# Performance work log

Measured on AMD Instinct MI355X. Metric: run time of the kernel, lower is better.

Reference implementation:

```python
import jax, jax.numpy as jnp
import numpy as np

B = 1024            # batch of CIFAR images (== number of routed tokens, seq_len is 1)
D = 768             # d_model (switch-base-8)
FF = 3072           # d_ff
E = 8               # num experts
L = 12              # encoder layers; odd-indexed layers are sparse MoE (sparse_step=2)
NM = L // 2         # 6 MoE layers and 6 dense FFN layers
NUM_CLASSES = 10


def setup_inputs() -> dict:
    key = jax.random.key(0)
    ks = jax.random.split(key, 12)
    s = 0.02
    return {
        "x": jax.random.normal(ks[0], (B, 3, 32, 32), jnp.float32),
        "proj_w": jax.random.normal(ks[1], (3 * 32 * 32, D), jnp.float32) * s,
        "proj_b": jnp.zeros((D,), jnp.float32),
        "ln1_w": jnp.ones((L, D), jnp.float32),
        "wv": jax.random.normal(ks[2], (L, D, D), jnp.float32) * s,
        "wo": jax.random.normal(ks[3], (L, D, D), jnp.float32) * s,
        "ln2_w": jnp.ones((L, D), jnp.float32),
        "dwi": jax.random.normal(ks[4], (NM, D, FF), jnp.float32) * s,
        "dwo": jax.random.normal(ks[5], (NM, FF, D), jnp.float32) * s,
        "router_w": jax.random.normal(ks[6], (NM, D, E), jnp.float32) * s,
        "ewi": jax.random.normal(ks[7], (NM, E, D, FF), jnp.float32) * s,
        "ewo": jax.random.normal(ks[8], (NM, E, FF, D), jnp.float32) * s,
        "final_ln_w": jnp.ones((D,), jnp.float32),
        "fc_w": jax.random.normal(ks[9], (D, NUM_CLASSES), jnp.float32) * s,
        "fc_b": jnp.zeros((NUM_CLASSES,), jnp.float32),
    }


def rms_norm(h, w, eps=1e-6):
    # T5LayerNorm: RMS norm, no mean subtraction, no bias
    var = jnp.mean(jnp.square(h), axis=-1, keepdims=True)
    return w * (h * jax.lax.rsqrt(var + eps))


def reference(x, proj_w, proj_b, ln1_w, wv, wo, ln2_w, dwi, dwo,
              router_w, ewi, ewo, final_ln_w, fc_w, fc_b):
    # flatten image, project to d_model; unsqueeze(1) in torch -> one token per image,
    # so we keep tokens as [B, D] throughout.
    h = x.reshape(x.shape[0], -1) @ proj_w + proj_b              # [B, D]
    d_i = 0
    m_i = 0
    for layer in range(L):
        # --- self-attention block. seq_len == 1 => softmax over a single key is
        #     identically 1 (for any scores / position bias), so the attention
        #     output is exactly Wo(Wv(x_norm)); q/k projections drop out of the
        #     math (and carry zero gradient).
        n = rms_norm(h, ln1_w[layer])
        h = h + (n @ wv[layer]) @ wo[layer]
        # --- feed-forward block (pre-norm, residual) ---
        n = rms_norm(h, ln2_w[layer])
        if layer % 2 == 1:
            # Switch top-1 MoE. With seq_len==1, token_priority==1 <= expert
            # capacity, so no tokens are ever dropped; every token goes to its
            # argmax expert and is scaled by the router probability.
            logits = n @ router_w[m_i]                           # [B, E]
            probs = jax.nn.softmax(logits, axis=-1)
            top_prob = jnp.max(probs, axis=-1, keepdims=True)    # [B, 1]
            disp = jax.nn.one_hot(jnp.argmax(probs, axis=-1), E, dtype=n.dtype)  # [B, E]
            # dense reference for the sparse dispatch: run every expert, then
            # combine with the one-hot routing mask (same math as gather/scatter)
            hid = jax.nn.relu(jnp.einsum('bd,edf->ebf', n, ewi[m_i]))   # [E, B, FF]
            eout = jnp.einsum('ebf,efd->ebd', hid, ewo[m_i])            # [E, B, D]
            moe = jnp.einsum('ebd,be->bd', eout, disp)                  # [B, D]
            h = h + top_prob * moe
            m_i += 1
        else:
            h = h + jax.nn.relu(n @ dwi[d_i]) @ dwo[d_i]
            d_i += 1
    h = rms_norm(h, final_ln_w)
    return h @ fc_w + fc_b                                      # [B, 10] logits
```

## Files before the change

### kernel.cpp

```cpp
#include <hip/hip_runtime.h>
#include <type_traits>

#define DEV __device__ __forceinline__

typedef _Float16 f16;
typedef __attribute__((ext_vector_type(8))) _Float16 f16x8;
typedef __attribute__((ext_vector_type(4))) float f32x4;

constexpr int NP = 48;

DEV int imin(int a, int b) { return a < b ? a : b; }

DEV int swz(int row, int colByte) { return (row * 128 + colByte) ^ ((row & 7) << 4); }

DEV void split2(float x, float y, unsigned& hi, unsigned& lo) {
  f16 hx = (f16)x, hy = (f16)y;
  f16 lx = (f16)(x - (float)hx), ly = (f16)(y - (float)hy);
  hi = (unsigned)__builtin_bit_cast(unsigned short, hx) |
       ((unsigned)__builtin_bit_cast(unsigned short, hy) << 16);
  lo = (unsigned)__builtin_bit_cast(unsigned short, lx) |
       ((unsigned)__builtin_bit_cast(unsigned short, ly) << 16);
}

DEV void lgkm_barrier() {
  asm volatile("s_waitcnt lgkmcnt(0)" ::: "memory");
  __builtin_amdgcn_s_barrier();
  asm volatile("" ::: "memory");
}

struct GArgs {
  const void* A; const void* Alo;
  const void* B; const void* Blo;
  const float* Hin; float* Hout;
  f16* O16; f16* O16lo;
  const float* rspIn; float* rspOut;
  const float* lnw;
  const int* perm; const int* off;
  int M, K, lda, ldb, ldo;
  long sAz, sBz, sOz;
  long zA, zB, zH;
  int KS;
};

template<int TM,int TN,int WR,int WC,int AM,int BMD,int CM,bool RESID,bool EXPERT>
DEV void gk_body(GArgs a) {
  constexpr int TK = 64;
  constexpr int NT = 256;
  static_assert(WR * WC == 4, "4 waves per block");
  constexpr int WTM = TM / WR, WTN = TN / WC;
  constexpr int FM = WTM / 16, FN = WTN / 16;
  constexpr bool APAIR = (AM == 0);
  constexpr int UA = APAIR ? (TM * (TK / 8)) / NT : (TM * (TK / 4)) / NT;
  constexpr int UB = (BMD == 0) ? (TN * (TK / 8)) / NT : (TN * (TK / 4)) / NT;

  __shared__ __align__(16) f16 As[2 * TM * TK];
  __shared__ __align__(16) f16 Bs[2 * TN * TK];
  __shared__ __align__(16) f16 AsL[2 * TM * TK];
  __shared__ __align__(16) f16 BsL[2 * TN * TK];
  __shared__ float rrlds[(AM == 2 || AM == 3) ? TM : 1];

  const int tid = threadIdx.x;
  const int lane = tid & 63;
  const int wid = tid >> 6;
  const int wr = wid / WC, wc = wid % WC;

  int m0;
  int sEnd = 0x7fffffff;
  const char* Ab = (const char*)a.A;
  const char* AbL = (const char*)a.Alo;
  const char* Bb = (const char*)a.B;
  const char* BbL = (const char*)a.Blo;
  f16* O = a.O16;
  f16* OL = a.O16lo;
  float* HoutP = a.Hout;
  {
    int z = blockIdx.z;
    int e = z / a.KS;
    int kc = z - e * a.KS;
    if constexpr (EXPERT) {
      int o0 = a.off[e], o1 = a.off[e + 1];
      if ((int)blockIdx.y * TM >= o1 - o0) return;
      m0 = o0 + blockIdx.y * TM;
      sEnd = o1;
      Bb += (long)e * a.sBz * 4 + (long)kc * a.zB;
      Ab += (long)kc * a.zA;
      AbL += (long)kc * a.zA;
    } else {
      m0 = blockIdx.y * TM;
      Ab += (long)e * a.sAz * 4 + (long)kc * a.zA;
      AbL += (long)kc * a.zA;
      Bb += (long)e * a.sBz * 4 + (long)kc * a.zB;
    }
    if constexpr (CM == 4) HoutP += (long)kc * a.zH;
  }
  const int n0 = blockIdx.x * TN;

  if constexpr (AM == 2 || AM == 3) {
    if (tid < TM) {
      int s = m0 + tid;
      int row = (AM == 3) ? a.perm[imin(s, a.M - 1)] : imin(s, a.M - 1);
      float ss = 0.f;
      #pragma unroll
      for (int j = 0; j < NP; ++j) ss += a.rspIn[row * NP + j];
      rrlds[tid] = rsqrtf(ss * (1.f / 768.f) + 1e-6f);
    }
  }

  int arow[UA];
  #pragma unroll
  for (int u = 0; u < UA; ++u) {
    int id = tid + u * NT;
    if constexpr (AM == 0) arow[u] = imin(m0 + (id >> 3), a.M - 1);
    else if constexpr (AM == 3) arow[u] = a.perm[imin(m0 + (id >> 4), a.M - 1)];
    else arow[u] = imin(m0 + (id >> 4), a.M - 1);
  }

  using ARt = typename std::conditional<APAIR, int4, float4>::type;
  using BRt = typename std::conditional<BMD == 0, int4, float4>::type;

  auto issueA = [&](ARt* rg, ARt* rl, int k0) {
    #pragma unroll
    for (int u = 0; u < UA; ++u) {
      int id = tid + u * NT;
      if constexpr (APAIR) {
        int kq = id & 7;
        long off = ((long)arow[u] * a.lda + k0 + kq * 8) * 2;
        rg[u] = *(const int4*)(Ab + off);
        rl[u] = *(const int4*)(AbL + off);
      } else {
        int kq = id & 15;
        rg[u] = *(const float4*)(Ab + ((long)arow[u] * a.lda + k0 + kq * 4) * 4);
      }
    }
  };
  auto commitA = [&](ARt* rg, ARt* rl, int k0, int bi) {
    char* base = (char*)As + bi * (TM * 128);
    char* baseL = (char*)AsL + bi * (TM * 128);
    #pragma unroll
    for (int u = 0; u < UA; ++u) {
      int id = tid + u * NT;
      if constexpr (APAIR) {
        int m = id >> 3, kq = id & 7;
        *(int4*)(base + swz(m, kq * 16)) = rg[u];
        *(int4*)(baseL + swz(m, kq * 16)) = rl[u];
      } else {
        int m = id >> 4, kq = id & 15;
        float4 v = *(float4*)&rg[u];
        if constexpr (AM == 2 || AM == 3) {
          float rr = rrlds[m];
          const float* w = a.lnw + k0 + kq * 4;
          v.x *= rr * w[0]; v.y *= rr * w[1]; v.z *= rr * w[2]; v.w *= rr * w[3];
        }
        uint2 ph, pl;
        split2(v.x, v.y, ph.x, pl.x);
        split2(v.z, v.w, ph.y, pl.y);
        *(uint2*)(base + swz(m, kq * 8)) = ph;
        *(uint2*)(baseL + swz(m, kq * 8)) = pl;
      }
    }
  };
  auto issueB = [&](BRt* rg, BRt* rl, int k0) {
    #pragma unroll
    for (int u = 0; u < UB; ++u) {
      int id = tid + u * NT;
      if constexpr (BMD == 0) {
        int n = id >> 3, kq = id & 7;
        long off = ((long)(n0 + n) * a.ldb + k0 + kq * 8) * 2;
        rg[u] = *(const int4*)(Bb + off);
        rl[u] = *(const int4*)(BbL + off);
      } else {
        int n = id % TN, kq = id / TN;
        const float* g = (const float*)Bb;
        #pragma unroll
        for (int i = 0; i < 4; ++i)
          ((float*)&rg[u])[i] = g[(long)(k0 + kq * 4 + i) * a.ldb + (n0 + n)];
      }
    }
  };
  auto commitB = [&](BRt* rg, BRt* rl, int bi) {
    char* base = (char*)Bs + bi * (TN * 128);
    char* baseL = (char*)BsL + bi * (TN * 128);
    #pragma unroll
    for (int u = 0; u < UB; ++u) {
      int id = tid + u * NT;
      if constexpr (BMD == 0) {
        int n = id >> 3, kq = id & 7;
        *(int4*)(base + swz(n, kq * 16)) = rg[u];
        *(int4*)(baseL + swz(n, kq * 16)) = rl[u];
      } else {
        int n = id % TN, kq = id / TN;
        float4 v = *(float4*)&rg[u];
        uint2 ph, pl;
        split2(v.x, v.y, ph.x, pl.x);
        split2(v.z, v.w, ph.y, pl.y);
        *(uint2*)(base + swz(n, kq * 8)) = ph;
        *(uint2*)(baseL + swz(n, kq * 8)) = pl;
      }
    }
  };

  f32x4 acc[FM][FN] = {};
  auto compute = [&](int bi) {
    const char* pA = (const char*)As + bi * (TM * 128);
    const char* pAL = (const char*)AsL + bi * (TM * 128);
    const char* pB = (const char*)Bs + bi * (TN * 128);
    const char* pBL = (const char*)BsL + bi * (TN * 128);
    #pragma unroll
    for (int kk = 0; kk < 2; ++kk) {
      const int col2 = (kk * 32 + (lane >> 4) * 8) * 2;
      f16x8 ah[FM], al[FM], bh[FN], bl[FN];
      #pragma unroll
      for (int i = 0; i < FM; ++i) {
        ah[i] = *(const f16x8*)(pA + swz(wr * WTM + i * 16 + (lane & 15), col2));
        al[i] = *(const f16x8*)(pAL + swz(wr * WTM + i * 16 + (lane & 15), col2));
      }
      #pragma unroll
      for (int j = 0; j < FN; ++j) {
        bh[j] = *(const f16x8*)(pB + swz(wc * WTN + j * 16 + (lane & 15), col2));
        bl[j] = *(const f16x8*)(pBL + swz(wc * WTN + j * 16 + (lane & 15), col2));
      }
      #pragma unroll
      for (int i = 0; i < FM; ++i)
        #pragma unroll
        for (int j = 0; j < FN; ++j) {
          f32x4 t = acc[i][j];
          t = __builtin_amdgcn_mfma_f32_16x16x32_f16(al[i], bh[j], t, 0, 0, 0);
          t = __builtin_amdgcn_mfma_f32_16x16x32_f16(ah[i], bl[j], t, 0, 0, 0);
          t = __builtin_amdgcn_mfma_f32_16x16x32_f16(ah[i], bh[j], t, 0, 0, 0);
          acc[i][j] = t;
        }
    }
  };

  ARt ag0[UA], ag1[UA], ag2[UA], al0[UA], al1[UA], al2[UA];
  BRt bg0[UB], bg1[UB], bg2[UB], bl0[UB], bl1[UB], bl2[UB];
  const int ns = a.K / TK;
  issueA(ag0, al0, 0); issueB(bg0, bl0, 0);
  if (TK < a.K) { issueA(ag1, al1, TK); issueB(bg1, bl1, TK); }
  __syncthreads();
  for (int s = 0; s < ns; s += 6) {
    int k;
    { commitA(ag0, al0, (s + 0) * TK, 0); commitB(bg0, bl0, 0);
      k = (s + 2) * TK; if (k < a.K) { issueA(ag2, al2, k); issueB(bg2, bl2, k); }
      lgkm_barrier(); compute(0); }
    if (s + 1 < ns) {
      commitA(ag1, al1, (s + 1) * TK, 1); commitB(bg1, bl1, 1);
      k = (s + 3) * TK; if (k < a.K) { issueA(ag0, al0, k); issueB(bg0, bl0, k); }
      lgkm_barrier(); compute(1); }
    if (s + 2 < ns) {
      commitA(ag2, al2, (s + 2) * TK, 0); commitB(bg2, bl2, 0);
      k = (s + 4) * TK; if (k < a.K) { issueA(ag1, al1, k); issueB(bg1, bl1, k); }
      lgkm_barrier(); compute(0); }
    if (s + 3 < ns) {
      commitA(ag0, al0, (s + 3) * TK, 1); commitB(bg0, bl0, 1);
      k = (s + 5) * TK; if (k < a.K) { issueA(ag2, al2, k); issueB(bg2, bl2, k); }
      lgkm_barrier(); compute(1); }
    if (s + 4 < ns) {
      commitA(ag1, al1, (s + 4) * TK, 0); commitB(bg1, bl1, 0);
      k = (s + 6) * TK; if (k < a.K) { issueA(ag0, al0, k); issueB(bg0, bl0, k); }
      lgkm_barrier(); compute(0); }
    if (s + 5 < ns) {
      commitA(ag2, al2, (s + 5) * TK, 1); commitB(bg2, bl2, 1);
      k = (s + 7) * TK; if (k < a.K) { issueA(ag1, al1, k); issueB(bg1, bl1, k); }
      lgkm_barrier(); compute(1); }
  }

  const int cr = (lane >> 4) * 4;
  const int cc = lane & 15;
  if constexpr (CM == 0 || CM == 2) {
    #pragma unroll
    for (int i = 0; i < FM; ++i) {
      #pragma unroll
      for (int r = 0; r < 4; ++r) {
        int gm = m0 + wr * WTM + i * 16 + cr + r;
        if (gm >= sEnd) continue;
        #pragma unroll
        for (int j = 0; j < FN; ++j) {
          int gn = n0 + wc * WTN + j * 16 + cc;
          float v = acc[i][j][r];
          if constexpr (CM == 2) v = fmaxf(v, 0.f);
          f16 hv = (f16)v;
          O[(long)gm * a.ldo + gn] = hv;
          OL[(long)gm * a.ldo + gn] = (f16)(v - (float)hv);
        }
      }
    }
  } else if constexpr (CM == 4) {
    #pragma unroll
    for (int i = 0; i < FM; ++i) {
      #pragma unroll
      for (int r = 0; r < 4; ++r) {
        int s = m0 + wr * WTM + i * 16 + cr + r;
        if (s >= sEnd || s >= a.M) continue;
        #pragma unroll
        for (int j = 0; j < FN; ++j) {
          int gn = n0 + wc * WTN + j * 16 + cc;
          HoutP[(long)s * a.ldo + gn] = acc[i][j][r];
        }
      }
    }
  } else {
    #pragma unroll
    for (int i = 0; i < FM; ++i) {
      #pragma unroll
      for (int r = 0; r < 4; ++r) {
        int gm = m0 + wr * WTM + i * 16 + cr + r;
        #pragma unroll
        for (int j = 0; j < FN; ++j) {
          int gn = n0 + wc * WTN + j * 16 + cc;
          float v = acc[i][j][r];
          if constexpr (RESID) v += a.Hin[(long)gm * 768 + gn];
          a.Hout[(long)gm * 768 + gn] = v;
          float ssum = v * v;
          ssum += __shfl_xor(ssum, 1); ssum += __shfl_xor(ssum, 2);
          ssum += __shfl_xor(ssum, 4); ssum += __shfl_xor(ssum, 8);
          if ((lane & 15) == 0)
            a.rspOut[(long)gm * NP + ((n0 + wc * WTN + j * 16) >> 4)] = ssum;
        }
      }
    }
  }
}

__global__ __launch_bounds__(256, 3) void k_wct(GArgs a)  { gk_body<32,64,2,2, 1,1,4, false,false>(a); }
__global__ __launch_bounds__(256, 3) void k_proj(GArgs a) { gk_body<32,64,2,2, 1,1,4, false,false>(a); }
__global__ __launch_bounds__(256, 3) void k_attn(GArgs a) { gk_body<32,32,2,2, 2,1,1, true, false>(a); }
__global__ __launch_bounds__(256, 3) void k_awv(GArgs a)  { gk_body<32,64,2,2, 2,1,0, false,false>(a); }
__global__ __launch_bounds__(256, 3) void k_awo(GArgs a)  { gk_body<32,64,2,2, 0,1,1, true, false>(a); }
__global__ __launch_bounds__(256, 3) void k_ffn1(GArgs a) { gk_body<32,64,2,2, 2,1,2, false,false>(a); }
__global__ __launch_bounds__(256, 3) void k_ffn2(GArgs a) { gk_body<32,64,2,2, 0,1,4, false,false>(a); }
__global__ __launch_bounds__(256, 3) void k_eg1(GArgs a)  { gk_body<64,32,2,2, 3,1,2, false,true>(a); }
__global__ __launch_bounds__(256, 3) void k_eg2(GArgs a)  { gk_body<32,64,2,2, 0,1,4, false,true>(a); }

__global__ __launch_bounds__(256)
void red_k(const float* slab, long sst, const int* perm, const float* prob,
           const float* Hin, const float* bias, float* Hout, float* rsp) {
  int lane = threadIdx.x & 63;
  int s = blockIdx.x * 4 + (threadIdx.x >> 6);
  int row = perm ? perm[s] : s;
  float p = prob ? prob[row] : 1.f;
  #pragma unroll
  for (int p3 = 0; p3 < 3; ++p3) {
    int c = p3 * 256 + lane * 4;
    float4 v = *(const float4*)(slab + (long)s * 768 + c);
    float4 v1 = *(const float4*)(slab + sst + (long)s * 768 + c);
    float4 v2 = *(const float4*)(slab + 2 * sst + (long)s * 768 + c);
    float4 v3 = *(const float4*)(slab + 3 * sst + (long)s * 768 + c);
    v.x = (v.x + v1.x) + (v2.x + v3.x); v.y = (v.y + v1.y) + (v2.y + v3.y);
    v.z = (v.z + v1.z) + (v2.z + v3.z); v.w = (v.w + v1.w) + (v2.w + v3.w);
    v.x *= p; v.y *= p; v.z *= p; v.w *= p;
    if (bias) {
      const float4 b = *(const float4*)(bias + c);
      v.x += b.x; v.y += b.y; v.z += b.z; v.w += b.w;
    }
    if (Hin) {
      const float4 h = *(const float4*)(Hin + (long)row * 768 + c);
      v.x += h.x; v.y += h.y; v.z += h.z; v.w += h.w;
    }
    *(float4*)(Hout + (long)row * 768 + c) = v;
    float ss = v.x * v.x + v.y * v.y + v.z * v.z + v.w * v.w;
    ss += __shfl_xor(ss, 1); ss += __shfl_xor(ss, 2);
    if ((lane & 3) == 0) rsp[(long)row * NP + p3 * 16 + (lane >> 2)] = ss;
  }
}

__global__ __launch_bounds__(256)
void router_k(const float* H, const float* rsp, const float* lnw, const float* rw,
              int* eid, float* prob) {
  int lane = threadIdx.x & 63;
  int row = blockIdx.x * 4 + (threadIdx.x >> 6);
  float ss = 0.f;
  #pragma unroll
  for (int j = 0; j < NP; ++j) ss += rsp[row * NP + j];
  float rr = rsqrtf(ss * (1.f / 768.f) + 1e-6f);
  float le[8] = {0, 0, 0, 0, 0, 0, 0, 0};
  #pragma unroll
  for (int i = 0; i < 12; ++i) {
    int k = i * 64 + lane;
    float n = H[row * 768 + k] * rr * lnw[k];
    const float* w = rw + k * 8;
    float4 w0 = *(const float4*)w, w1 = *(const float4*)(w + 4);
    le[0] += n * w0.x; le[1] += n * w0.y; le[2] += n * w0.z; le[3] += n * w0.w;
    le[4] += n * w1.x; le[5] += n * w1.y; le[6] += n * w1.z; le[7] += n * w1.w;
  }
  #pragma unroll
  for (int m = 1; m < 64; m <<= 1) {
    #pragma unroll
    for (int e = 0; e < 8; ++e) le[e] += __shfl_xor(le[e], m);
  }
  float mx = le[0]; int am = 0;
  #pragma unroll
  for (int e = 1; e < 8; ++e) if (le[e] > mx) { mx = le[e]; am = e; }
  float den = 0.f;
  #pragma unroll
  for (int e = 0; e < 8; ++e) den += expf(le[e] - mx);
  if (lane == 0) { eid[row] = am; prob[row] = 1.f / den; }
}

__global__ __launch_bounds__(256)
void scan_k(const int* eid, int* off, int* perm) {
  __shared__ int cnt[8], c2[8], offs[9];
  int tid = threadIdx.x;
  if (tid < 8) { cnt[tid] = 0; c2[tid] = 0; }
  __syncthreads();
  for (int t = tid; t < 1024; t += 256) atomicAdd(&cnt[eid[t]], 1);
  __syncthreads();
  if (tid == 0) {
    int acc = 0;
    for (int e = 0; e < 8; ++e) { offs[e] = acc; acc += cnt[e]; }
    offs[8] = acc;
    for (int e = 0; e < 9; ++e) off[e] = offs[e];
  }
  __syncthreads();
  for (int t = tid; t < 1024; t += 256) {
    int e = eid[t];
    int r = atomicAdd(&c2[e], 1);
    perm[offs[e] + r] = t;
  }
}

__global__ __launch_bounds__(256)
void fc_k(const float* H, const float* rsp, const float* lnw, const float* fw,
          const float* fb, float* out) {
  int lane = threadIdx.x & 63;
  int row = blockIdx.x * 4 + (threadIdx.x >> 6);
  float ss = 0.f;
  #pragma unroll
  for (int j = 0; j < NP; ++j) ss += rsp[row * NP + j];
  float rr = rsqrtf(ss * (1.f / 768.f) + 1e-6f);
  float acc[10] = {0, 0, 0, 0, 0, 0, 0, 0, 0, 0};
  #pragma unroll
  for (int i = 0; i < 12; ++i) {
    int k = i * 64 + lane;
    float n = H[row * 768 + k] * rr * lnw[k];
    const float* w = fw + k * 10;
    #pragma unroll
    for (int c = 0; c < 10; ++c) acc[c] += n * w[c];
  }
  #pragma unroll
  for (int m = 1; m < 64; m <<= 1) {
    #pragma unroll
    for (int c = 0; c < 10; ++c) acc[c] += __shfl_xor(acc[c], m);
  }
  if (lane == 0) {
    #pragma unroll
    for (int c = 0; c < 10; ++c) out[row * 10 + c] = acc[c] + fb[c];
  }
}

extern "C" void kernel_launch(void* const* d_in, const int* in_sizes, int n_in,
                              void* d_out, int out_size, void* d_ws, size_t ws_size,
                              hipStream_t stream) {
  const float* x     = (const float*)d_in[0];
  const float* projw = (const float*)d_in[1];
  const float* projb = (const float*)d_in[2];
  const float* ln1   = (const float*)d_in[3];
  const float* wvp   = (const float*)d_in[4];
  const float* wop   = (const float*)d_in[5];
  const float* ln2   = (const float*)d_in[6];
  const float* dwi   = (const float*)d_in[7];
  const float* dwo   = (const float*)d_in[8];
  const float* rw    = (const float*)d_in[9];
  const float* ewi   = (const float*)d_in[10];
  const float* ewo   = (const float*)d_in[11];
  const float* flnw  = (const float*)d_in[12];
  const float* fcw   = (const float*)d_in[13];
  const float* fcb   = (const float*)d_in[14];

  char* ws = (char*)d_ws;
  float* hA   = (float*)(ws);
  float* hB   = (float*)(ws + 3145728);
  f16*   hidH = (f16*)(ws + 6291456);
  f16*   hidL = (f16*)(ws + 12582912);
  float* rsp  = (float*)(ws + 18874368);
  int*   eid  = (int*)(ws + 23789568);
  float* prob = (float*)(ws + 23793664);
  int*   perm = (int*)(ws + 23797760);
  int*   off  = (int*)(ws + 23801856);
  float* slab = (float*)(ws + 23802368);
  float* wct  = (float*)(ws + 36385280);
  if (ws_size < 36385280u) return;
  const bool useWct = ws_size >= 64696832u;
  auto slot = [&](int s) { return rsp + (long)s * 1024 * NP; };
  const long SST = 1024 * 768;

  if (useWct) {
    GArgs g{}; g.A = wvp; g.B = wop; g.Hout = wct; g.KS = 12;
    g.M = 768; g.K = 768; g.lda = 768; g.ldb = 768; g.ldo = 768;
    g.zA = (long)589824 * 4; g.zB = (long)589824 * 4; g.zH = 589824;
    k_wct<<<dim3(12,24,12), 256, 0, stream>>>(g);
  }
  {
    GArgs g{}; g.A = x; g.B = projw; g.Hout = slab; g.KS = 4;
    g.M = 1024; g.K = 768; g.lda = 3072; g.ldb = 768; g.ldo = 768;
    g.zA = 768 * 4; g.zB = (long)768 * 768 * 4; g.zH = SST;
    k_proj<<<dim3(12,32,4), 256, 0, stream>>>(g);
    red_k<<<dim3(256), 256, 0, stream>>>(slab, SST, nullptr, nullptr, nullptr, projb, hA, slot(0));
  }
  for (int l = 0; l < 12; ++l) {
    if (useWct) {
      GArgs g{}; g.A = hA; g.B = wct + (long)l * 589824;
      g.Hin = hA; g.Hout = hB; g.KS = 1;
      g.rspIn = slot(2*l); g.rspOut = slot(2*l+1); g.lnw = ln1 + l * 768;
      g.M = 1024; g.K = 768; g.lda = 768; g.ldb = 768;
      k_attn<<<dim3(24,32,1), 256, 0, stream>>>(g);
    } else {
      {
        GArgs g{}; g.A = hA; g.B = wvp + (long)l * 589824;
        g.O16 = hidH; g.O16lo = hidL; g.KS = 1;
        g.rspIn = slot(2*l); g.lnw = ln1 + l * 768;
        g.M = 1024; g.K = 768; g.lda = 768; g.ldb = 768; g.ldo = 768;
        k_awv<<<dim3(12,32,1), 256, 0, stream>>>(g);
      }
      {
        GArgs g{}; g.A = hidH; g.Alo = hidL; g.B = wop + (long)l * 589824;
        g.Hin = hA; g.Hout = hB; g.rspOut = slot(2*l+1); g.KS = 1;
        g.M = 1024; g.K = 768; g.lda = 768; g.ldb = 768;
        k_awo<<<dim3(12,32,1), 256, 0, stream>>>(g);
      }
    }
    if ((l & 1) == 0) {
      int di = l / 2;
      {
        GArgs g{}; g.A = hB; g.B = dwi + (long)di * 768 * 3072;
        g.O16 = hidH; g.O16lo = hidL; g.KS = 1;
        g.rspIn = slot(2*l+1); g.lnw = ln2 + l * 768;
        g.M = 1024; g.K = 768; g.lda = 768; g.ldb = 3072; g.ldo = 3072;
        k_ffn1<<<dim3(48,32,1), 256, 0, stream>>>(g);
      }
      {
        GArgs g{}; g.A = hidH; g.Alo = hidL; g.B = dwo + (long)di * 3072 * 768;
        g.Hout = slab; g.KS = 4;
        g.M = 1024; g.K = 768; g.lda = 3072; g.ldb = 768; g.ldo = 768;
        g.zA = 768 * 2; g.zB = (long)768 * 768 * 4; g.zH = SST;
        k_ffn2<<<dim3(12,32,4), 256, 0, stream>>>(g);
        red_k<<<dim3(256), 256, 0, stream>>>(slab, SST, nullptr, nullptr, hB, nullptr, hA, slot(2*l+2));
      }
    } else {
      int mi = l / 2;
      router_k<<<dim3(256), 256, 0, stream>>>(hB, slot(2*l+1), ln2 + l * 768,
                                              rw + (long)mi * 768 * 8, eid, prob);
      scan_k<<<dim3(1), 256, 0, stream>>>(eid, off, perm);
      {
        GArgs g{}; g.A = hB; g.B = ewi + (long)mi * 8 * 768 * 3072;
        g.O16 = hidH; g.O16lo = hidL; g.perm = perm; g.off = off; g.KS = 1;
        g.rspIn = slot(2*l+1); g.lnw = ln2 + l * 768;
        g.M = 1024; g.K = 768; g.lda = 768; g.ldb = 3072; g.ldo = 3072;
        g.sBz = (long)768 * 3072;
        k_eg1<<<dim3(96,16,8), 256, 0, stream>>>(g);
      }
      {
        GArgs g{}; g.A = hidH; g.Alo = hidL; g.B = ewo + (long)mi * 8 * 3072 * 768;
        g.Hout = slab; g.off = off; g.KS = 4;
        g.M = 1024; g.K = 768; g.lda = 3072; g.ldb = 768; g.ldo = 768;
        g.sBz = (long)3072 * 768; g.zA = 768 * 2; g.zB = (long)768 * 768 * 4; g.zH = SST;
        k_eg2<<<dim3(12,32,32), 256, 0, stream>>>(g);
        red_k<<<dim3(256), 256, 0, stream>>>(slab, SST, perm, prob, hB, nullptr, hA, slot(2*l+2));
      }
    }
  }
  fc_k<<<dim3(256), 256, 0, stream>>>(hA, slot(24), flnw, fcw, fcb, (float*)d_out);
}
```

Baseline: 1.750 ms.

## Drop split-K slabs and fuse reductions, routing scan into GEMM epilogues

The projection, dense FFN2 and expert FFN2 GEMMs no longer use 4-way split-K with a partial-sum slab and a separate red_k reduction. They now run full K in one pass, and bias, router-probability scaling, permuted scatter and residual add are applied directly in the GEMM epilogue. The router and scan kernels are merged into one kernel, where the last block to finish (tracked by an atomic ticket) does the expert histogram and permutation. This removes launches and slab memory traffic. In exchange, the affected GEMMs get 4x fewer blocks with 4x longer K loops, which can hurt occupancy and parallelism on a GPU with many CUs.

```diff
diff --git a/kernel.cpp b/kernel.cpp
--- a/kernel.cpp
+++ b/kernel.cpp
@@ -35,6 +35,7 @@
   f16* O16; f16* O16lo;
   const float* rspIn; float* rspOut;
   const float* lnw;
+  const float* prob; const float* bias;
   const int* perm; const int* off;
   int M, K, lda, ldb, ldo;
   long sAz, sBz, sOz;
@@ -42,7 +43,7 @@
   int KS;
 };
 
-template<int TM,int TN,int WR,int WC,int AM,int BMD,int CM,bool RESID,bool EXPERT>
+template<int TM,int TN,int WR,int WC,int AM,int BMD,int CM,bool RESID,bool BIAS,bool EXPERT>
 DEV void gk_body(GArgs a) {
   constexpr int TK = 64;
   constexpr int NT = 256;
@@ -51,7 +52,7 @@
   constexpr int FM = WTM / 16, FN = WTN / 16;
   constexpr bool APAIR = (AM == 0);
   constexpr int UA = APAIR ? (TM * (TK / 8)) / NT : (TM * (TK / 4)) / NT;
-  constexpr int UB = (BMD == 0) ? (TN * (TK / 8)) / NT : (TN * (TK / 4)) / NT;
+  constexpr int UB = (TN * (TK / 4)) / NT;
 
   __shared__ __align__(16) f16 As[2 * TM * TK];
   __shared__ __align__(16) f16 Bs[2 * TN * TK];
@@ -69,7 +70,6 @@
   const char* Ab = (const char*)a.A;
   const char* AbL = (const char*)a.Alo;
   const char* Bb = (const char*)a.B;
-  const char* BbL = (const char*)a.Blo;
   f16* O = a.O16;
   f16* OL = a.O16lo;
   float* HoutP = a.Hout;
@@ -116,7 +116,7 @@
   }
 
   using ARt = typename std::conditional<APAIR, int4, float4>::type;
-  using BRt = typename std::conditional<BMD == 0, int4, float4>::type;
+  using BRt = float4;
 
   auto issueA = [&](ARt* rg, ARt* rl, int k0) {
     #pragma unroll
@@ -159,43 +159,30 @@
       }
     }
   };
-  auto issueB = [&](BRt* rg, BRt* rl, int k0) {
+  auto issueB = [&](BRt* rg, int k0) {
     #pragma unroll
     for (int u = 0; u < UB; ++u) {
       int id = tid + u * NT;
-      if constexpr (BMD == 0) {
-        int n = id >> 3, kq = id & 7;
-        long off = ((long)(n0 + n) * a.ldb + k0 + kq * 8) * 2;
-        rg[u] = *(const int4*)(Bb + off);
-        rl[u] = *(const int4*)(BbL + off);
-      } else {
-        int n = id % TN, kq = id / TN;
-        const float* g = (const float*)Bb;
-        #pragma unroll
-        for (int i = 0; i < 4; ++i)
-          ((float*)&rg[u])[i] = g[(long)(k0 + kq * 4 + i) * a.ldb + (n0 + n)];
-      }
+      int n = id % TN, kq = id / TN;
+      const float* g = (const float*)Bb;
+      #pragma unroll
+      for (int i = 0; i < 4; ++i)
+        ((float*)&rg[u])[i] = g[(long)(k0 + kq * 4 + i) * a.ldb + (n0 + n)];
     }
   };
-  auto commitB = [&](BRt* rg, BRt* rl, int bi) {
+  auto commitB = [&](BRt* rg, int bi) {
     char* base = (char*)Bs + bi * (TN * 128);
     char* baseL = (char*)BsL + bi * (TN * 128);
     #pragma unroll
     for (int u = 0; u < UB; ++u) {
       int id = tid + u * NT;
-      if constexpr (BMD == 0) {
-        int n = id >> 3, kq = id & 7;
-        *(int4*)(base + swz(n, kq * 16)) = rg[u];
-        *(int4*)(baseL + swz(n, kq * 16)) = rl[u];
-      } else {
-        int n = id % TN, kq = id / TN;
-        float4 v = *(float4*)&rg[u];
-        uint2 ph, pl;
-        split2(v.x, v.y, ph.x, pl.x);
-        split2(v.z, v.w, ph.y, pl.y);
-        *(uint2*)(base + swz(n, kq * 8)) = ph;
-        *(uint2*)(baseL + swz(n, kq * 8)) = pl;
-      }
+      int n = id % TN, kq = id / TN;
+      float4 v = *(float4*)&rg[u];
+      uint2 ph, pl;
+      split2(v.x, v.y, ph.x, pl.x);
+      split2(v.z, v.w, ph.y, pl.y);
+      *(uint2*)(base + swz(n, kq * 8)) = ph;
+      *(uint2*)(baseL + swz(n, kq * 8)) = pl;
     }
   };
 
@@ -233,35 +220,35 @@
   };
 
   ARt ag0[UA], ag1[UA], ag2[UA], al0[UA], al1[UA], al2[UA];
-  BRt bg0[UB], bg1[UB], bg2[UB], bl0[UB], bl1[UB], bl2[UB];
+  BRt bg0[UB], bg1[UB], bg2[UB];
   const int ns = a.K / TK;
-  issueA(ag0, al0, 0); issueB(bg0, bl0, 0);
-  if (TK < a.K) { issueA(ag1, al1, TK); issueB(bg1, bl1, TK); }
+  issueA(ag0, al0, 0); issueB(bg0, 0);
+  if (TK < a.K) { issueA(ag1, al1, TK); issueB(bg1, TK); }
   __syncthreads();
   for (int s = 0; s < ns; s += 6) {
     int k;
-    { commitA(ag0, al0, (s + 0) * TK, 0); commitB(bg0, bl0, 0);
-      k = (s + 2) * TK; if (k < a.K) { issueA(ag2, al2, k); issueB(bg2, bl2, k); }
+    { commitA(ag0, al0, (s + 0) * TK, 0); commitB(bg0, 0);
+      k = (s + 2) * TK; if (k < a.K) { issueA(ag2, al2, k); issueB(bg2, k); }
       lgkm_barrier(); compute(0); }
     if (s + 1 < ns) {
-      commitA(ag1, al1, (s + 1) * TK, 1); commitB(bg1, bl1, 1);
-      k = (s + 3) * TK; if (k < a.K) { issueA(ag0, al0, k); issueB(bg0, bl0, k); }
+      commitA(ag1, al1, (s + 1) * TK, 1); commitB(bg1, 1);
+      k = (s + 3) * TK; if (k < a.K) { issueA(ag0, al0, k); issueB(bg0, k); }
       lgkm_barrier(); compute(1); }
     if (s + 2 < ns) {
-      commitA(ag2, al2, (s + 2) * TK, 0); commitB(bg2, bl2, 0);
-      k = (s + 4) * TK; if (k < a.K) { issueA(ag1, al1, k); issueB(bg1, bl1, k); }
+      commitA(ag2, al2, (s + 2) * TK, 0); commitB(bg2, 0);
+      k = (s + 4) * TK; if (k < a.K) { issueA(ag1, al1, k); issueB(bg1, k); }
       lgkm_barrier(); compute(0); }
     if (s + 3 < ns) {
-      commitA(ag0, al0, (s + 3) * TK, 1); commitB(bg0, bl0, 1);
-      k = (s + 5) * TK; if (k < a.K) { issueA(ag2, al2, k); issueB(bg2, bl2, k); }
+      commitA(ag0, al0, (s + 3) * TK, 1); commitB(bg0, 1);
+      k = (s + 5) * TK; if (k < a.K) { issueA(ag2, al2, k); issueB(bg2, k); }
       lgkm_barrier(); compute(1); }
     if (s + 4 < ns) {
-      commitA(ag1, al1, (s + 4) * TK, 0); commitB(bg1, bl1, 0);
-      k = (s + 6) * TK; if (k < a.K) { issueA(ag0, al0, k); issueB(bg0, bl0, k); }
+      commitA(ag1, al1, (s + 4) * TK, 0); commitB(bg1, 0);
+      k = (s + 6) * TK; if (k < a.K) { issueA(ag0, al0, k); issueB(bg0, k); }
       lgkm_barrier(); compute(0); }
     if (s + 5 < ns) {
-      commitA(ag2, al2, (s + 5) * TK, 1); commitB(bg2, bl2, 1);
-      k = (s + 7) * TK; if (k < a.K) { issueA(ag1, al1, k); issueB(bg1, bl1, k); }
+      commitA(ag2, al2, (s + 5) * TK, 1); commitB(bg2, 1);
+      k = (s + 7) * TK; if (k < a.K) { issueA(ag1, al1, k); issueB(bg1, k); }
       lgkm_barrier(); compute(1); }
   }
 
@@ -304,71 +291,50 @@
     for (int i = 0; i < FM; ++i) {
       #pragma unroll
       for (int r = 0; r < 4; ++r) {
-        int gm = m0 + wr * WTM + i * 16 + cr + r;
+        int s = m0 + wr * WTM + i * 16 + cr + r;
+        int grow = s;
+        float p = 1.f;
+        bool ok = true;
+        if constexpr (CM == 3) {
+          ok = s < sEnd;
+          int t = a.perm[imin(s, a.M - 1)];
+          grow = t;
+          p = a.prob[t];
+        }
         #pragma unroll
         for (int j = 0; j < FN; ++j) {
           int gn = n0 + wc * WTN + j * 16 + cc;
           float v = acc[i][j][r];
-          if constexpr (RESID) v += a.Hin[(long)gm * 768 + gn];
-          a.Hout[(long)gm * 768 + gn] = v;
+          if constexpr (CM == 3) v *= p;
+          if constexpr (BIAS) v += a.bias[gn];
+          if constexpr (RESID) v += a.Hin[(long)grow * 768 + gn];
+          if constexpr (CM == 3) v += a.Hin[(long)grow * 768 + gn];
+          if (ok) a.Hout[(long)grow * 768 + gn] = v;
           float ssum = v * v;
           ssum += __shfl_xor(ssum, 1); ssum += __shfl_xor(ssum, 2);
           ssum += __shfl_xor(ssum, 4); ssum += __shfl_xor(ssum, 8);
-          if ((lane & 15) == 0)
-            a.rspOut[(long)gm * NP + ((n0 + wc * WTN + j * 16) >> 4)] = ssum;
+          if (ok && (lane & 15) == 0)
+            a.rspOut[(long)grow * NP + ((n0 + wc * WTN + j * 16) >> 4)] = ssum;
         }
       }
     }
   }
 }
 
-__global__ __launch_bounds__(256, 3) void k_wct(GArgs a)  { gk_body<32,64,2,2, 1,1,4, false,false>(a); }
-__global__ __launch_bounds__(256, 3) void k_proj(GArgs a) { gk_body<32,64,2,2, 1,1,4, false,false>(a); }
-__global__ __launch_bounds__(256, 3) void k_attn(GArgs a) { gk_body<32,32,2,2, 2,1,1, true, false>(a); }
-__global__ __launch_bounds__(256, 3) void k_awv(GArgs a)  { gk_body<32,64,2,2, 2,1,0, false,false>(a); }
-__global__ __launch_bounds__(256, 3) void k_awo(GArgs a)  { gk_body<32,64,2,2, 0,1,1, true, false>(a); }
-__global__ __launch_bounds__(256, 3) void k_ffn1(GArgs a) { gk_body<32,64,2,2, 2,1,2, false,false>(a); }
-__global__ __launch_bounds__(256, 3) void k_ffn2(GArgs a) { gk_body<32,64,2,2, 0,1,4, false,false>(a); }
-__global__ __launch_bounds__(256, 3) void k_eg1(GArgs a)  { gk_body<64,32,2,2, 3,1,2, false,true>(a); }
-__global__ __launch_bounds__(256, 3) void k_eg2(GArgs a)  { gk_body<32,64,2,2, 0,1,4, false,true>(a); }
+__global__ __launch_bounds__(256, 3) void k_wct(GArgs a)  { gk_body<32,64,2,2, 1,1,4, false,false,false>(a); }
+__global__ __launch_bounds__(256, 3) void k_proj(GArgs a) { gk_body<32,64,2,2, 1,1,1, false,true, false>(a); }
+__global__ __launch_bounds__(256, 3) void k_attn(GArgs a) { gk_body<32,32,2,2, 2,1,1, true, false,false>(a); }
+__global__ __launch_bounds__(256, 3) void k_ffn1(GArgs a) { gk_body<32,64,2,2, 2,1,2, false,false,false>(a); }
+__global__ __launch_bounds__(256, 3) void k_ffn2(GArgs a) { gk_body<32,64,2,2, 0,1,1, true, false,false>(a); }
+__global__ __launch_bounds__(256, 3) void k_eg1(GArgs a)  { gk_body<64,32,2,2, 3,1,2, false,false,true>(a); }
+__global__ __launch_bounds__(256, 3) void k_eg2(GArgs a)  { gk_body<32,64,2,2, 0,1,3, false,false,true>(a); }
 
 __global__ __launch_bounds__(256)
-void red_k(const float* slab, long sst, const int* perm, const float* prob,
-           const float* Hin, const float* bias, float* Hout, float* rsp) {
-  int lane = threadIdx.x & 63;
-  int s = blockIdx.x * 4 + (threadIdx.x >> 6);
-  int row = perm ? perm[s] : s;
-  float p = prob ? prob[row] : 1.f;
-  #pragma unroll
-  for (int p3 = 0; p3 < 3; ++p3) {
-    int c = p3 * 256 + lane * 4;
-    float4 v = *(const float4*)(slab + (long)s * 768 + c);
-    float4 v1 = *(const float4*)(slab + sst + (long)s * 768 + c);
-    float4 v2 = *(const float4*)(slab + 2 * sst + (long)s * 768 + c);
-    float4 v3 = *(const float4*)(slab + 3 * sst + (long)s * 768 + c);
-    v.x = (v.x + v1.x) + (v2.x + v3.x); v.y = (v.y + v1.y) + (v2.y + v3.y);
-    v.z = (v.z + v1.z) + (v2.z + v3.z); v.w = (v.w + v1.w) + (v2.w + v3.w);
-    v.x *= p; v.y *= p; v.z *= p; v.w *= p;
-    if (bias) {
-      const float4 b = *(const float4*)(bias + c);
-      v.x += b.x; v.y += b.y; v.z += b.z; v.w += b.w;
-    }
-    if (Hin) {
-      const float4 h = *(const float4*)(Hin + (long)row * 768 + c);
-      v.x += h.x; v.y += h.y; v.z += h.z; v.w += h.w;
-    }
-    *(float4*)(Hout + (long)row * 768 + c) = v;
-    float ss = v.x * v.x + v.y * v.y + v.z * v.z + v.w * v.w;
-    ss += __shfl_xor(ss, 1); ss += __shfl_xor(ss, 2);
-    if ((lane & 3) == 0) rsp[(long)row * NP + p3 * 16 + (lane >> 2)] = ss;
-  }
-}
-
-__global__ __launch_bounds__(256)
-void router_k(const float* H, const float* rsp, const float* lnw, const float* rw,
-              int* eid, float* prob) {
-  int lane = threadIdx.x & 63;
-  int row = blockIdx.x * 4 + (threadIdx.x >> 6);
+void rs_k(const float* H, const float* rsp, const float* lnw, const float* rw,
+          int* eid, float* prob, int* off, int* perm, int* done) {
+  int tid = threadIdx.x;
+  int lane = tid & 63;
+  int row = blockIdx.x * 4 + (tid >> 6);
   float ss = 0.f;
   #pragma unroll
   for (int j = 0; j < NP; ++j) ss += rsp[row * NP + j];
@@ -388,28 +354,31 @@
     #pragma unroll
     for (int e = 0; e < 8; ++e) le[e] += __shfl_xor(le[e], m);
   }
-  float mx = le[0]; int am = 0;
-  #pragma unroll
-  for (int e = 1; e < 8; ++e) if (le[e] > mx) { mx = le[e]; am = e; }
-  float den = 0.f;
-  #pragma unroll
-  for (int e = 0; e < 8; ++e) den += expf(le[e] - mx);
-  if (lane == 0) { eid[row] = am; prob[row] = 1.f / den; }
-}
-
-__global__ __launch_bounds__(256)
-void scan_k(const int* eid, int* off, int* perm) {
+  if (lane == 0) {
+    float mx = le[0]; int am = 0;
+    #pragma unroll
+    for (int e = 1; e < 8; ++e) if (le[e] > mx) { mx = le[e]; am = e; }
+    float den = 0.f;
+    #pragma unroll
+    for (int e = 0; e < 8; ++e) den += expf(le[e] - mx);
+    eid[row] = am; prob[row] = 1.f / den;
+  }
+  __threadfence();
+  __shared__ int ticket;
+  if (tid == 0) ticket = atomicAdd(done, 1);
+  __syncthreads();
+  if (ticket != (int)gridDim.x - 1) return;
+  __threadfence();
   __shared__ int cnt[8], c2[8], offs[9];
-  int tid = threadIdx.x;
   if (tid < 8) { cnt[tid] = 0; c2[tid] = 0; }
   __syncthreads();
   for (int t = tid; t < 1024; t += 256) atomicAdd(&cnt[eid[t]], 1);
   __syncthreads();
   if (tid == 0) {
     int acc = 0;
-    for (int e = 0; e < 8; ++e) { offs[e] = acc; acc += cnt[e]; }
-    offs[8] = acc;
-    for (int e = 0; e < 9; ++e) off[e] = offs[e];
+    for (int e = 0; e < 8; ++e) { offs[e] = acc; off[e] = acc; acc += cnt[e]; }
+    offs[8] = acc; off[8] = acc;
+    *done = 0;
   }
   __syncthreads();
   for (int t = tid; t < 1024; t += 256) {
@@ -477,12 +446,13 @@
   float* prob = (float*)(ws + 23793664);
   int*   perm = (int*)(ws + 23797760);
   int*   off  = (int*)(ws + 23801856);
-  float* slab = (float*)(ws + 23802368);
+  int*   done = (int*)(ws + 23802112);
   float* wct  = (float*)(ws + 36385280);
   if (ws_size < 36385280u) return;
   const bool useWct = ws_size >= 64696832u;
   auto slot = [&](int s) { return rsp + (long)s * 1024 * NP; };
-  const long SST = 1024 * 768;
+
+  hipMemsetAsync(done, 0, 4, stream);
 
   if (useWct) {
     GArgs g{}; g.A = wvp; g.B = wop; g.Hout = wct; g.KS = 12;
@@ -491,11 +461,9 @@
     k_wct<<<dim3(12,24,12), 256, 0, stream>>>(g);
   }
   {
-    GArgs g{}; g.A = x; g.B = projw; g.Hout = slab; g.KS = 4;
-    g.M = 1024; g.K = 768; g.lda = 3072; g.ldb = 768; g.ldo = 768;
-    g.zA = 768 * 4; g.zB = (long)768 * 768 * 4; g.zH = SST;
-    k_proj<<<dim3(12,32,4), 256, 0, stream>>>(g);
-    red_k<<<dim3(256), 256, 0, stream>>>(slab, SST, nullptr, nullptr, nullptr, projb, hA, slot(0));
+    GArgs g{}; g.A = x; g.B = projw; g.Hout = hA; g.bias = projb; g.rspOut = slot(0); g.KS = 1;
+    g.M = 1024; g.K = 3072; g.lda = 3072; g.ldb = 768; g.ldo = 768;
+    k_proj<<<dim3(12,32,1), 256, 0, stream>>>(g);
   }
   for (int l = 0; l < 12; ++l) {
     if (useWct) {
@@ -510,13 +478,13 @@
         g.O16 = hidH; g.O16lo = hidL; g.KS = 1;
         g.rspIn = slot(2*l); g.lnw = ln1 + l * 768;
         g.M = 1024; g.K = 768; g.lda = 768; g.ldb = 768; g.ldo = 768;
-        k_awv<<<dim3(12,32,1), 256, 0, stream>>>(g);
+        k_ffn1<<<dim3(12,32,1), 256, 0, stream>>>(g);
       }
       {
         GArgs g{}; g.A = hidH; g.Alo = hidL; g.B = wop + (long)l * 589824;
         g.Hin = hA; g.Hout = hB; g.rspOut = slot(2*l+1); g.KS = 1;
         g.M = 1024; g.K = 768; g.lda = 768; g.ldb = 768;
-        k_awo<<<dim3(12,32,1), 256, 0, stream>>>(g);
+        k_ffn2<<<dim3(12,32,1), 256, 0, stream>>>(g);
       }
     }
     if ((l & 1) == 0) {
@@ -530,17 +498,14 @@
       }
       {
         GArgs g{}; g.A = hidH; g.Alo = hidL; g.B = dwo + (long)di * 3072 * 768;
-        g.Hout = slab; g.KS = 4;
-        g.M = 1024; g.K = 768; g.lda = 3072; g.ldb = 768; g.ldo = 768;
-        g.zA = 768 * 2; g.zB = (long)768 * 768 * 4; g.zH = SST;
-        k_ffn2<<<dim3(12,32,4), 256, 0, stream>>>(g);
-        red_k<<<dim3(256), 256, 0, stream>>>(slab, SST, nullptr, nullptr, hB, nullptr, hA, slot(2*l+2));
+        g.Hin = hB; g.Hout = hA; g.rspOut = slot(2*l+2); g.KS = 1;
+        g.M = 1024; g.K = 3072; g.lda = 3072; g.ldb = 768;
+        k_ffn2<<<dim3(12,32,1), 256, 0, stream>>>(g);
       }
     } else {
       int mi = l / 2;
-      router_k<<<dim3(256), 256, 0, stream>>>(hB, slot(2*l+1), ln2 + l * 768,
-                                              rw + (long)mi * 768 * 8, eid, prob);
-      scan_k<<<dim3(1), 256, 0, stream>>>(eid, off, perm);
+      rs_k<<<dim3(256), 256, 0, stream>>>(hB, slot(2*l+1), ln2 + l * 768,
+                                          rw + (long)mi * 768 * 8, eid, prob, off, perm, done);
       {
         GArgs g{}; g.A = hB; g.B = ewi + (long)mi * 8 * 768 * 3072;
         g.O16 = hidH; g.O16lo = hidL; g.perm = perm; g.off = off; g.KS = 1;
@@ -551,11 +516,11 @@
       }
       {
         GArgs g{}; g.A = hidH; g.Alo = hidL; g.B = ewo + (long)mi * 8 * 3072 * 768;
-        g.Hout = slab; g.off = off; g.KS = 4;
-        g.M = 1024; g.K = 768; g.lda = 3072; g.ldb = 768; g.ldo = 768;
-        g.sBz = (long)3072 * 768; g.zA = 768 * 2; g.zB = (long)768 * 768 * 4; g.zH = SST;
-        k_eg2<<<dim3(12,32,32), 256, 0, stream>>>(g);
-        red_k<<<dim3(256), 256, 0, stream>>>(slab, SST, perm, prob, hB, nullptr, hA, slot(2*l+2));
+        g.Hin = hB; g.Hout = hA; g.rspOut = slot(2*l+2);
+        g.perm = perm; g.prob = prob; g.off = off; g.KS = 1;
+        g.M = 1024; g.K = 3072; g.lda = 3072; g.ldb = 768;
+        g.sBz = (long)3072 * 768;
+        k_eg2<<<dim3(12,32,8), 256, 0, stream>>>(g);
       }
     }
   }
```

New measurement: 2.006 ms. 14.6% more time.
